# Performance work log

Hardware: AMD Instinct MI355X
Metric: run time of the kernel (lower is better)

## Reference

```python
import jax, jax.numpy as jnp
import numpy as np

S = 2          # scale_int = ceil(scale)
K = 3          # kernel size
OUTC = 3       # num_out_ch
NUM_FEAT = 64


def conv3x3(x, w, b):
    y = jax.lax.conv_general_dilated(x, w, (1, 1), ((1, 1), (1, 1)),
                                     dimension_numbers=('NCHW', 'OIHW', 'NCHW'))
    return y + b[None, :, None, None]


def unfold3x3(x):
    # torch F.unfold(x, 3, padding=1): (N, C*9, H*W), order c*9 + ki*3 + kj
    N, C, H, W = x.shape
    xp = jnp.pad(x, ((0, 0), (0, 0), (1, 1), (1, 1)))
    patches = jnp.stack([xp[:, :, i:i + H, j:j + W]
                         for i in range(3) for j in range(3)], axis=2)  # (N,C,9,H,W)
    return patches.reshape(N, C * 9, H * W)


def setup_inputs() -> dict:
    key = jax.random.key(0)
    ks = jax.random.split(key, 12)
    b, t, c, h, w = 2, 4, 16, 64, 64
    H, W = S * h, S * w
    nf4 = 64 // 4  # 16
    d_w = K * K * NUM_FEAT * OUTC  # 1728
    return {
        'x0': jax.random.normal(ks[0], (b, NUM_FEAT, h, w), jnp.float32),
        'feature': jax.random.normal(ks[1], (b, t, c, h, w), jnp.float32),
        'pos_mat': jax.random.uniform(ks[2], (H, W, 3), jnp.float32),
        'mask': jnp.ones((b, OUTC, H, W), dtype=bool),
        'conv1_w': jax.random.normal(ks[3], (nf4, 64, 3, 3), jnp.float32) * 0.05,
        'conv1_b': jnp.zeros((nf4,), jnp.float32),
        'conv2_w': jax.random.normal(ks[4], (nf4, nf4, 3, 3), jnp.float32) * 0.05,
        'conv2_b': jnp.zeros((nf4,), jnp.float32),
        'f2w1_w': jax.random.normal(ks[5], (256, nf4 + 1), jnp.float32) * 0.05,
        'f2w1_b': jnp.zeros((256,), jnp.float32),
        'f2w2_w': jax.random.normal(ks[6], (d_w, 256), jnp.float32) * 0.05,
        'f2w2_b': jnp.zeros((d_w,), jnp.float32),
    }


def reference(x0, feature, pos_mat, mask, conv1_w, conv1_b, conv2_w, conv2_b,
              f2w1_w, f2w1_b, f2w2_w, f2w2_b):
    b, t, c, h, w = feature.shape
    H, W = S * h, S * w
    # with_gradBack=False -> feature.detach()
    feat = jax.lax.stop_gradient(feature).reshape(b, t * c, h, w)
    # repeat_x(..., upsample=True): nearest-neighbour upsample by S
    feat_up = jnp.repeat(jnp.repeat(feat, S, axis=2), S, axis=3)  # (b,64,H,W)
    f = jax.nn.relu(conv3x3(feat_up, conv1_w, conv1_b))
    f = conv3x3(f, conv2_w, conv2_b)                              # (b,16,H,W)
    pos0 = jnp.transpose(pos_mat, (2, 0, 1))[0:1]                 # (1,H,W)
    fm = jnp.concatenate([f, jnp.broadcast_to(pos0[None], (b, 1, H, W))], axis=1)
    fm = fm.reshape(b, -1, H * W).transpose(0, 2, 1)              # (b,HW,17)
    hdn = jax.nn.relu(fm @ f2w1_w.T + f2w1_b)
    weights = hdn @ f2w2_w.T + f2w2_b                             # (b,HW,1728)
    weights = weights.reshape(b, h, S, w, S, K * K * NUM_FEAT, OUTC)
    weights = jnp.transpose(weights, (0, 2, 4, 1, 3, 5, 6))
    weights = weights.reshape(b, S * S, h * w, K * K * NUM_FEAT, OUTC)
    # repeat_x(x0) tiles x0 S^2 times -> all S^2 col copies identical; compute once
    cols = unfold3x3(x0).transpose(0, 2, 1)                       # (b,hw,576)
    out = jnp.einsum('bpk,bspko->bspo', cols, weights)            # (b,S^2,hw,3)
    out = jnp.transpose(out, (0, 1, 3, 2)).reshape(b, S, S, OUTC, h, w)
    out = jnp.transpose(out, (0, 3, 4, 1, 5, 2)).reshape(b, OUTC, H, W)
    # integer scale -> mask all True -> masked_select + view is identity
    return out, weights
```

## Files before the change

kernel.cpp:

```cpp
#include <hip/hip_runtime.h>

#define THREADS 256

#define Bsz 2
#define HWp 16384
#define Ntot (Bsz*HWp)
#define HID 256
#define Mm 1728
#define FMC 17
#define W_OFF 98304

#define F1_OFF  0
#define F1_SZ   (Bsz*16*HWp)
#define FM_OFF  F1_SZ
#define WB2_OFF (FM_OFF + Ntot*FMC)

typedef __attribute__((ext_vector_type(8))) short bf16x8;
typedef __attribute__((ext_vector_type(4))) float f32x4;

static __device__ __forceinline__ short f2bf(float x) {
    unsigned u = __builtin_bit_cast(unsigned, x);
    unsigned r = (u + 0x7fff + ((u >> 16) & 1)) >> 16;
    return (short)r;
}

__global__ __launch_bounds__(THREADS) void k13_conv1_cvt(const float* __restrict__ feat,
                                                         const float* __restrict__ w1,
                                                         const float* __restrict__ b1,
                                                         float* __restrict__ f1,
                                                         const float* __restrict__ w2g,
                                                         short* __restrict__ wB2) {
    int tid = threadIdx.x;
    if (blockIdx.x >= 256) {
        int t = (blockIdx.x - 256) * THREADS + tid;
        int i = t & 7, l = (t >> 3) & 63, ct = (t >> 9) & 3, s = (t >> 11) & 7, mc = t >> 14;
        int col = mc * 64 + ct * 16 + (l & 15);
        int k = s * 32 + (l >> 4) * 8 + i;
        wB2[t] = f2bf(w2g[col * HID + k]);
        return;
    }
    __shared__ float sW[4 * 64 * 4];
    int b = blockIdx.x;
    int rb = b & 7, oc = (b >> 3) & 15, bb = b >> 7;
    int c = tid & 63, sr = tid >> 6;
    int r0 = rb * 4 + sr;
    int r1 = r0 + 32;

    #pragma unroll
    for (int q = 0; q < 4; ++q) {
        int e = tid * 4 + q;
        int v = e & 1, u = (e >> 1) & 1, ic = (e >> 2) & 63, pp = (e >> 8) & 3;
        int pi = pp >> 1, pj = pp & 1;
        float s = 0.f;
        for (int ki = 0; ki < 3; ++ki) {
            bool okki = pi ? (u ? (ki == 2) : (ki <= 1)) : (u ? (ki >= 1) : (ki == 0));
            if (!okki) continue;
            for (int kj = 0; kj < 3; ++kj) {
                bool okkj = pj ? (v ? (kj == 2) : (kj <= 1)) : (v ? (kj >= 1) : (kj == 0));
                if (okkj) s += w1[((oc * 64 + ic) * 3 + ki) * 3 + kj];
            }
        }
        sW[(pp * 64 + ic) * 4 + u * 2 + v] = s;
    }
    __syncthreads();

    float bias = b1[oc];
    float aA00 = bias, aA01 = bias, aA10 = bias, aA11 = bias;
    float aB00 = bias, aB01 = bias, aB10 = bias, aB11 = bias;

    float mA = (r0 > 0) ? 1.f : 0.f;
    float mB = (r1 < 63) ? 1.f : 0.f;
    float mc0 = (c > 0) ? 1.f : 0.f, mc2 = (c < 63) ? 1.f : 0.f;
    int roA0 = (r0 > 0) ? -64 : 0;
    int roB2 = (r1 < 63) ? 64 : 0;
    int co0 = (c > 0) ? -1 : 0, co2 = (c < 63) ? 1 : 0;

    const float* fbA = feat + bb * 64 * 4096 + r0 * 64 + c;
    const float* fbB = feat + bb * 64 * 4096 + r1 * 64 + c;
    for (int ic = 0; ic < 64; ++ic) {
        const float* pA1 = fbA + ic * 4096;
        const float* pA0 = pA1 + roA0;
        const float* pA2 = pA1 + 64;
        const float* pB1 = fbB + ic * 4096;
        const float* pB0 = pB1 - 64;
        const float* pB2 = pB1 + roB2;

        float vA00 = pA0[co0] * (mA * mc0), vA01 = pA0[0] * mA, vA02 = pA0[co2] * (mA * mc2);
        float vA10 = pA1[co0] * mc0,        vA11 = pA1[0],      vA12 = pA1[co2] * mc2;
        float vA20 = pA2[co0] * mc0,        vA21 = pA2[0],      vA22 = pA2[co2] * mc2;
        float vB00 = pB0[co0] * mc0,        vB01 = pB0[0],      vB02 = pB0[co2] * mc2;
        float vB10 = pB1[co0] * mc0,        vB11 = pB1[0],      vB12 = pB1[co2] * mc2;
        float vB20 = pB2[co0] * (mB * mc0), vB21 = pB2[0] * mB, vB22 = pB2[co2] * (mB * mc2);

        f32x4 w0 = *(const f32x4*)(sW + (0 * 64 + ic) * 4);
        f32x4 w1v = *(const f32x4*)(sW + (1 * 64 + ic) * 4);
        f32x4 w2v = *(const f32x4*)(sW + (2 * 64 + ic) * 4);
        f32x4 w3 = *(const f32x4*)(sW + (3 * 64 + ic) * 4);

        aA00 = fmaf(w0[0], vA00, aA00); aA00 = fmaf(w0[1], vA01, aA00);
        aA00 = fmaf(w0[2], vA10, aA00); aA00 = fmaf(w0[3], vA11, aA00);
        aA01 = fmaf(w1v[0], vA01, aA01); aA01 = fmaf(w1v[1], vA02, aA01);
        aA01 = fmaf(w1v[2], vA11, aA01); aA01 = fmaf(w1v[3], vA12, aA01);
        aA10 = fmaf(w2v[0], vA10, aA10); aA10 = fmaf(w2v[1], vA11, aA10);
        aA10 = fmaf(w2v[2], vA20, aA10); aA10 = fmaf(w2v[3], vA21, aA10);
        aA11 = fmaf(w3[0], vA11, aA11); aA11 = fmaf(w3[1], vA12, aA11);
        aA11 = fmaf(w3[2], vA21, aA11); aA11 = fmaf(w3[3], vA22, aA11);

        aB00 = fmaf(w0[0], vB00, aB00); aB00 = fmaf(w0[1], vB01, aB00);
        aB00 = fmaf(w0[2], vB10, aB00); aB00 = fmaf(w0[3], vB11, aB00);
        aB01 = fmaf(w1v[0], vB01, aB01); aB01 = fmaf(w1v[1], vB02, aB01);
        aB01 = fmaf(w1v[2], vB11, aB01); aB01 = fmaf(w1v[3], vB12, aB01);
        aB10 = fmaf(w2v[0], vB10, aB10); aB10 = fmaf(w2v[1], vB11, aB10);
        aB10 = fmaf(w2v[2], vB20, aB10); aB10 = fmaf(w2v[3], vB21, aB10);
        aB11 = fmaf(w3[0], vB11, aB11); aB11 = fmaf(w3[1], vB12, aB11);
        aB11 = fmaf(w3[2], vB21, aB11); aB11 = fmaf(w3[3], vB22, aB11);
    }

    float* foA = f1 + (bb * 16 + oc) * HWp + (2 * r0) * 128 + 2 * c;
    *reinterpret_cast<float2*>(foA)       = make_float2(fmaxf(aA00, 0.f), fmaxf(aA01, 0.f));
    *reinterpret_cast<float2*>(foA + 128) = make_float2(fmaxf(aA10, 0.f), fmaxf(aA11, 0.f));
    float* foB = f1 + (bb * 16 + oc) * HWp + (2 * r1) * 128 + 2 * c;
    *reinterpret_cast<float2*>(foB)       = make_float2(fmaxf(aB00, 0.f), fmaxf(aB01, 0.f));
    *reinterpret_cast<float2*>(foB + 128) = make_float2(fmaxf(aB10, 0.f), fmaxf(aB11, 0.f));
}

__global__ __launch_bounds__(THREADS) void k2_conv2_fm(const float* __restrict__ f1,
                                                       const float* __restrict__ w2,
                                                       const float* __restrict__ b2,
                                                       const float* __restrict__ pos,
                                                       float* __restrict__ fm) {
    int tid = threadIdx.x;
    int t = blockIdx.x * THREADS + tid;
    int J = t & 127, I = (t >> 7) & 127, h = (t >> 14) & 1, bb = t >> 15;

    float acc[8];
    #pragma unroll
    for (int o = 0; o < 8; ++o) acc[o] = b2[h * 8 + o];

    int ro0 = (I > 0) ? -128 : 0, ro2 = (I < 127) ? 128 : 0;
    int co0 = (J > 0) ? -1 : 0, co2 = (J < 127) ? 1 : 0;
    float mr0 = (I > 0) ? 1.f : 0.f, mr2 = (I < 127) ? 1.f : 0.f;
    float mcl = (J > 0) ? 1.f : 0.f, mcr = (J < 127) ? 1.f : 0.f;

    const float* fb = f1 + bb * 16 * HWp + I * 128 + J;
    #pragma unroll 4
    for (int ic = 0; ic < 16; ++ic) {
        const float* p1 = fb + ic * HWp;
        const float* p0 = p1 + ro0;
        const float* p2 = p1 + ro2;
        float v0 = p0[co0] * (mr0 * mcl), v1 = p0[0] * mr0, v2 = p0[co2] * (mr0 * mcr);
        float v3 = p1[co0] * mcl,         v4 = p1[0],       v5 = p1[co2] * mcr;
        float v6 = p2[co0] * (mr2 * mcl), v7 = p2[0] * mr2, v8 = p2[co2] * (mr2 * mcr);
        const float* wp = w2 + (h * 8 * 16 + ic) * 9;
        #pragma unroll
        for (int o = 0; o < 8; ++o) {
            const float* w = wp + o * 144;
            acc[o] = fmaf(v0, w[0], acc[o]); acc[o] = fmaf(v1, w[1], acc[o]);
            acc[o] = fmaf(v2, w[2], acc[o]); acc[o] = fmaf(v3, w[3], acc[o]);
            acc[o] = fmaf(v4, w[4], acc[o]); acc[o] = fmaf(v5, w[5], acc[o]);
            acc[o] = fmaf(v6, w[6], acc[o]); acc[o] = fmaf(v7, w[7], acc[o]);
            acc[o] = fmaf(v8, w[8], acc[o]);
        }
    }
    int n = bb * HWp + I * 128 + J;
    #pragma unroll
    for (int o = 0; o < 8; ++o) fm[n * FMC + h * 8 + o] = acc[o];
    if (h == 0) fm[n * FMC + 16] = pos[(I * 128 + J) * 3];
}

__global__ __launch_bounds__(THREADS, 2) void k4_gemm(const float* __restrict__ fm,
                                                      const float* __restrict__ w1g,
                                                      const float* __restrict__ b1g,
                                                      const short* __restrict__ wB2,
                                                      const float* __restrict__ b2g,
                                                      const float* __restrict__ x0g,
                                                      float* __restrict__ dout) {
    __shared__ short    sA[16384];
    __shared__ float    sFM[64 * 20];
    __shared__ int      sOB[64];
    __shared__ float    sX[6528];
    __shared__ unsigned sLUT[1792];
    __shared__ float    sOut[4 * 64 * 3];

    int tid = threadIdx.x;
    int n0 = blockIdx.x * 64;
    int bb = n0 >> 14, tt = n0 & 16383, I = tt >> 7, J0 = tt & 127;
    int i0 = I >> 1, jmin = J0 >> 1;

    for (int idx = tid; idx < 64 * FMC; idx += THREADS) {
        int r = idx / FMC, i2 = idx - r * FMC;
        sFM[r * 20 + i2] = fm[n0 * FMC + idx];
    }
    if (tid < 64) {
        int J = J0 + tid;
        int s = ((I & 1) << 1) | (J & 1);
        int p = ((I >> 1) << 6) | (J >> 1);
        sOB[tid] = W_OFF + ((bb * 4 + s) * 4096 + p) * Mm;
    }
    for (int m = tid; m < Mm; m += THREADS) {
        int k = m / 3;
        int ch = k / 9, rem = k - ch * 9;
        int ki = rem / 3, kj = rem - ki * 3;
        sLUT[m] = (unsigned)((ch * 3 + ki) * 34 + kj);
    }
    {
        const float* x0b = x0g + bb * 64 * 4096;
        for (int e = tid; e < 6528; e += THREADS) {
            int ch = e / 102, r2 = e - ch * 102;
            int ki = r2 / 34, jc = r2 - ki * 34;
            int y = i0 + ki - 1, x = jmin + jc - 1;
            float v = 0.f;
            if ((unsigned)y < 64u && (unsigned)x < 64u) v = x0b[(ch * 64 + y) * 64 + x];
            sX[e] = v;
        }
    }
    __syncthreads();

    {
        float wreg[FMC];
        #pragma unroll
        for (int i = 0; i < FMC; ++i) wreg[i] = w1g[tid * FMC + i];
        float bj = b1g[tid];
        int g = (tid >> 3) & 7;
        int base = (tid >> 3) * 512 + (tid & 7);
        for (int rr = 0; rr < 64; ++rr) {
            int r = (rr + g) & 63;
            const float* fr = sFM + r * 20;
            f32x4 x0 = *(const f32x4*)fr;
            f32x4 x1 = *(const f32x4*)(fr + 4);
            f32x4 x2 = *(const f32x4*)(fr + 8);
            f32x4 x3 = *(const f32x4*)(fr + 12);
            float s = fmaf(fr[16], wreg[16], bj);
            s = fmaf(x0[0], wreg[0], s);  s = fmaf(x0[1], wreg[1], s);
            s = fmaf(x0[2], wreg[2], s);  s = fmaf(x0[3], wreg[3], s);
            s = fmaf(x1[0], wreg[4], s);  s = fmaf(x1[1], wreg[5], s);
            s = fmaf(x1[2], wreg[6], s);  s = fmaf(x1[3], wreg[7], s);
            s = fmaf(x2[0], wreg[8], s);  s = fmaf(x2[1], wreg[9], s);
            s = fmaf(x2[2], wreg[10], s); s = fmaf(x2[3], wreg[11], s);
            s = fmaf(x3[0], wreg[12], s); s = fmaf(x3[1], wreg[13], s);
            s = fmaf(x3[2], wreg[14], s); s = fmaf(x3[3], wreg[15], s);
            sA[base + r * 8] = f2bf(fmaxf(s, 0.f));
        }
    }
    __syncthreads();

    int wid = tid >> 6, l = tid & 63;
    int lm = l & 15, lg = l >> 4;
    int lg3 = lg % 3;

    int pixbase[4], jl[4];
    #pragma unroll
    for (int rt = 0; rt < 4; ++rt) {
        pixbase[rt] = sOB[rt * 16 + lm];
        jl[rt] = rt * 8 + (lm >> 1);
    }

    const short* aptr = sA + lg * 512 + lm * 8;

    float racc[4][3];
    #pragma unroll
    for (int rt = 0; rt < 4; ++rt) {
        racc[rt][0] = 0.f; racc[rt][1] = 0.f; racc[rt][2] = 0.f;
    }

    for (int mc = wid; mc < 27; mc += 4) {
        int m0 = mc * 64;
        f32x4 acc[4][4];
        #pragma unroll
        for (int ct = 0; ct < 4; ++ct) {
            f32x4 bias4 = *(const f32x4*)(b2g + m0 + ct * 16 + lg * 4);
            #pragma unroll
            for (int rt = 0; rt < 4; ++rt)
                acc[rt][ct] = bias4;
        }
        const short* bbase = wB2 + (size_t)mc * 16384 + l * 8;
        #pragma unroll 2
        for (int s = 0; s < 8; ++s) {
            bf16x8 af[4], bfr[4];
            #pragma unroll
            for (int rt = 0; rt < 4; ++rt)
                af[rt] = *(const bf16x8*)(aptr + s * 2048 + rt * 128);
            #pragma unroll
            for (int ct = 0; ct < 4; ++ct)
                bfr[ct] = *(const bf16x8*)(bbase + (s * 4 + ct) * 512);
            #pragma unroll
            for (int rt = 0; rt < 4; ++rt)
                #pragma unroll
                for (int ct = 0; ct < 4; ++ct)
                    acc[rt][ct] = __builtin_amdgcn_mfma_f32_16x16x32_bf16(
                        bfr[ct], af[rt], acc[rt][ct], 0, 0, 0);
        }
        #pragma unroll
        for (int rt = 0; rt < 4; ++rt)
            #pragma unroll
            for (int ct = 0; ct < 4; ++ct)
                *(f32x4*)(dout + pixbase[rt] + m0 + ct * 16 + lg * 4) = acc[rt][ct];
        unsigned lutv[4];
#define ACCUM(QB)                                                              \
        _Pragma("unroll")                                                      \
        for (int ct = 0; ct < 4; ++ct) {                                       \
            *(uint4*)lutv = *(const uint4*)(sLUT + m0 + ct * 16 + lg * 4);     \
            _Pragma("unroll")                                                  \
            for (int r = 0; r < 4; ++r) {                                      \
                _Pragma("unroll")                                              \
                for (int rt = 0; rt < 4; ++rt) {                               \
                    float v = sX[lutv[r] + jl[rt]];                            \
                    racc[rt][((QB) + ct + r) % 3] =                            \
                        fmaf(acc[rt][ct][r], v, racc[rt][((QB) + ct + r) % 3]);\
                }                                                              \
            }                                                                  \
        }
        switch (mc % 3) {
            case 0: ACCUM(0); break;
            case 1: ACCUM(1); break;
            default: ACCUM(2); break;
        }
#undef ACCUM
    }

    #pragma unroll
    for (int rt = 0; rt < 4; ++rt) {
        float q0 = racc[rt][0], q1 = racc[rt][1], q2 = racc[rt][2];
        float a0 = (lg3 == 0) ? q0 : ((lg3 == 1) ? q2 : q1);
        float a1 = (lg3 == 0) ? q1 : ((lg3 == 1) ? q0 : q2);
        float a2 = (lg3 == 0) ? q2 : ((lg3 == 1) ? q1 : q0);
        a0 += __shfl_xor(a0, 16, 64); a0 += __shfl_xor(a0, 32, 64);
        a1 += __shfl_xor(a1, 16, 64); a1 += __shfl_xor(a1, 32, 64);
        a2 += __shfl_xor(a2, 16, 64); a2 += __shfl_xor(a2, 32, 64);
        if (l < 16) {
            float* so = sOut + (wid * 64 + rt * 16 + lm) * 3;
            so[0] = a0; so[1] = a1; so[2] = a2;
        }
    }
    __syncthreads();
    if (tid < 192) {
        float s = sOut[tid] + sOut[192 + tid] + sOut[384 + tid] + sOut[576 + tid];
        int pix = tid / 3, o = tid - 3 * pix;
        dout[bb * 3 * HWp + o * HWp + I * 128 + J0 + pix] = s;
    }
}

extern "C" void kernel_launch(void* const* d_in, const int* in_sizes, int n_in,
                              void* d_out, int out_size, void* d_ws, size_t ws_size,
                              hipStream_t stream) {
    const float* x0      = (const float*)d_in[0];
    const float* feature = (const float*)d_in[1];
    const float* pos     = (const float*)d_in[2];
    const float* w1      = (const float*)d_in[4];
    const float* b1      = (const float*)d_in[5];
    const float* w2      = (const float*)d_in[6];
    const float* b2      = (const float*)d_in[7];
    const float* f2w1_w  = (const float*)d_in[8];
    const float* f2w1_b  = (const float*)d_in[9];
    const float* f2w2_w  = (const float*)d_in[10];
    const float* f2w2_b  = (const float*)d_in[11];

    float* out = (float*)d_out;
    float* ws  = (float*)d_ws;
    float* f1  = ws + F1_OFF;
    float* fm  = ws + FM_OFF;
    short* wB2 = (short*)(ws + WB2_OFF);

    k13_conv1_cvt<<<256 + 1728, THREADS, 0, stream>>>(feature, w1, b1, f1, f2w2_w, wB2);
    k2_conv2_fm<<<(Bsz * 2 * HWp) / THREADS, THREADS, 0, stream>>>(f1, w2, b2, pos, fm);
    k4_gemm<<<Ntot / 64, THREADS, 0, stream>>>(fm, f2w1_w, f2w1_b, wB2, f2w2_b, x0, out);
}
```

Before: 123.8 us.

## Split hidden layer into separate MFMA kernel staging bf16 activations in output buffer

Moves the first MLP layer (17->256 with ReLU) out of the main GEMM kernel into a new kernel that uses bf16 MFMA with a pre-converted, zero-padded weight tile. The bf16 hidden activations are written into the weights region of the output buffer as scratch and reloaded by the GEMM kernel with vector copies. The GEMM kernel also drops its LUT and restructures the x0 patch tile into a transposed layout, so the unfold indices are computed arithmetically with two loads per four outputs. This adds a kernel launch and a global round trip for the hidden activations. It depends on each block reading its scratch before other blocks overwrite that region, and the first-layer inputs and weights are now rounded to bf16.

```diff
diff --git a/kernel.cpp b/kernel.cpp
--- a/kernel.cpp
+++ b/kernel.cpp
@@ -14,6 +14,7 @@
 #define F1_SZ   (Bsz*16*HWp)
 #define FM_OFF  F1_SZ
 #define WB2_OFF (FM_OFF + Ntot*FMC)
+#define WB1_OFF (WB2_OFF + (Mm*HID)/2)
 
 typedef __attribute__((ext_vector_type(8))) short bf16x8;
 typedef __attribute__((ext_vector_type(4))) float f32x4;
@@ -29,8 +30,18 @@
                                                          const float* __restrict__ b1,
                                                          float* __restrict__ f1,
                                                          const float* __restrict__ w2g,
-                                                         short* __restrict__ wB2) {
+                                                         short* __restrict__ wB2,
+                                                         const float* __restrict__ w1g,
+                                                         short* __restrict__ wB1) {
     int tid = threadIdx.x;
+    if (blockIdx.x >= 1984) {
+        for (int idx = tid; idx < 8192; idx += THREADS) {
+            int i = idx & 7, l = (idx >> 3) & 63, h = idx >> 9;
+            int k = (l >> 4) * 8 + i, hid = h * 16 + (l & 15);
+            wB1[idx] = (k < FMC) ? f2bf(w1g[hid * FMC + k]) : (short)0;
+        }
+        return;
+    }
     if (blockIdx.x >= 256) {
         int t = (blockIdx.x - 256) * THREADS + tid;
         int i = t & 7, l = (t >> 3) & 63, ct = (t >> 9) & 3, s = (t >> 11) & 7, mc = t >> 14;
@@ -168,40 +179,71 @@
     if (h == 0) fm[n * FMC + 16] = pos[(I * 128 + J) * 3];
 }
 
-__global__ __launch_bounds__(THREADS, 2) void k4_gemm(const float* __restrict__ fm,
-                                                      const float* __restrict__ w1g,
-                                                      const float* __restrict__ b1g,
-                                                      const short* __restrict__ wB2,
+__global__ __launch_bounds__(THREADS) void k35_hdn(const float* __restrict__ fm,
+                                                   const short* __restrict__ wB1,
+                                                   const float* __restrict__ b1g,
+                                                   float* __restrict__ dout) {
+    int tid = threadIdx.x;
+    int n0 = blockIdx.x * 64;
+    int bb = n0 >> 14, tt = n0 & 16383, I = tt >> 7, J0 = tt & 127;
+    int s0 = (I & 1) * 2, i0 = I >> 1, jmin = J0 >> 1;
+    short* sp = (short*)(dout + (size_t)W_OFF +
+                         ((size_t)(bb * 4 + s0) * 4096 + i0 * 64 + jmin) * Mm);
+
+    int w = tid >> 6, l = tid & 63, lm = l & 15, lg = l >> 4;
+    int row = w * 16 + lm;
+    const float* fr = fm + (n0 + row) * FMC;
+    bf16x8 af;
+    #pragma unroll
+    for (int i = 0; i < 8; ++i) {
+        int k = lg * 8 + i;
+        float x = (k < FMC) ? fr[k] : 0.f;
+        af[i] = f2bf(x);
+    }
+    const short* wb = wB1 + l * 8;
+    int pbase = ((lg >> 1) * 64 + row) * 8 + (lg & 1) * 4;
+    #pragma unroll 4
+    for (int h = 0; h < 16; ++h) {
+        bf16x8 bfr = *(const bf16x8*)(wb + h * 512);
+        f32x4 bias = *(const f32x4*)(b1g + h * 16 + lg * 4);
+        f32x4 acc = __builtin_amdgcn_mfma_f32_16x16x32_bf16(bfr, af, bias, 0, 0, 0);
+        unsigned c0 = (unsigned short)f2bf(fmaxf(acc[0], 0.f));
+        unsigned c1 = (unsigned short)f2bf(fmaxf(acc[1], 0.f));
+        unsigned c2 = (unsigned short)f2bf(fmaxf(acc[2], 0.f));
+        unsigned c3 = (unsigned short)f2bf(fmaxf(acc[3], 0.f));
+        uint2 uv; uv.x = c0 | (c1 << 16); uv.y = c2 | (c3 << 16);
+        *(uint2*)(sp + pbase + h * 1024) = uv;
+    }
+}
+
+__global__ __launch_bounds__(THREADS, 2) void k4_gemm(const short* __restrict__ wB2,
                                                       const float* __restrict__ b2g,
                                                       const float* __restrict__ x0g,
                                                       float* __restrict__ dout) {
-    __shared__ short    sA[16384];
-    __shared__ float    sFM[64 * 20];
-    __shared__ int      sOB[64];
-    __shared__ float    sX[6528];
-    __shared__ unsigned sLUT[1792];
-    __shared__ float    sOut[4 * 64 * 3];
+    __shared__ short sA[16384];
+    __shared__ int   sOB[64];
+    __shared__ float sXT[6632];
+    __shared__ float sOut[4 * 64 * 3];
 
     int tid = threadIdx.x;
     int n0 = blockIdx.x * 64;
     int bb = n0 >> 14, tt = n0 & 16383, I = tt >> 7, J0 = tt & 127;
-    int i0 = I >> 1, jmin = J0 >> 1;
-
-    for (int idx = tid; idx < 64 * FMC; idx += THREADS) {
-        int r = idx / FMC, i2 = idx - r * FMC;
-        sFM[r * 20 + i2] = fm[n0 * FMC + idx];
+    int s0 = (I & 1) * 2, i0 = I >> 1, jmin = J0 >> 1;
+
+    {
+        const short* spc = (const short*)(dout + (size_t)W_OFF +
+                             ((size_t)(bb * 4 + s0) * 4096 + i0 * 64 + jmin) * Mm);
+        #pragma unroll
+        for (int q = 0; q < 8; ++q) {
+            int si = (q * 256 + tid) * 8;
+            *(bf16x8*)(sA + si) = *(const bf16x8*)(spc + si);
+        }
     }
     if (tid < 64) {
         int J = J0 + tid;
         int s = ((I & 1) << 1) | (J & 1);
         int p = ((I >> 1) << 6) | (J >> 1);
         sOB[tid] = W_OFF + ((bb * 4 + s) * 4096 + p) * Mm;
-    }
-    for (int m = tid; m < Mm; m += THREADS) {
-        int k = m / 3;
-        int ch = k / 9, rem = k - ch * 9;
-        int ki = rem / 3, kj = rem - ki * 3;
-        sLUT[m] = (unsigned)((ch * 3 + ki) * 34 + kj);
     }
     {
         const float* x0b = x0g + bb * 64 * 4096;
@@ -211,48 +253,20 @@
             int y = i0 + ki - 1, x = jmin + jc - 1;
             float v = 0.f;
             if ((unsigned)y < 64u && (unsigned)x < 64u) v = x0b[(ch * 64 + y) * 64 + x];
-            sX[e] = v;
-        }
-    }
-    __syncthreads();
-
-    {
-        float wreg[FMC];
-        #pragma unroll
-        for (int i = 0; i < FMC; ++i) wreg[i] = w1g[tid * FMC + i];
-        float bj = b1g[tid];
-        int g = (tid >> 3) & 7;
-        int base = (tid >> 3) * 512 + (tid & 7);
-        for (int rr = 0; rr < 64; ++rr) {
-            int r = (rr + g) & 63;
-            const float* fr = sFM + r * 20;
-            f32x4 x0 = *(const f32x4*)fr;
-            f32x4 x1 = *(const f32x4*)(fr + 4);
-            f32x4 x2 = *(const f32x4*)(fr + 8);
-            f32x4 x3 = *(const f32x4*)(fr + 12);
-            float s = fmaf(fr[16], wreg[16], bj);
-            s = fmaf(x0[0], wreg[0], s);  s = fmaf(x0[1], wreg[1], s);
-            s = fmaf(x0[2], wreg[2], s);  s = fmaf(x0[3], wreg[3], s);
-            s = fmaf(x1[0], wreg[4], s);  s = fmaf(x1[1], wreg[5], s);
-            s = fmaf(x1[2], wreg[6], s);  s = fmaf(x1[3], wreg[7], s);
-            s = fmaf(x2[0], wreg[8], s);  s = fmaf(x2[1], wreg[9], s);
-            s = fmaf(x2[2], wreg[10], s); s = fmaf(x2[3], wreg[11], s);
-            s = fmaf(x3[0], wreg[12], s); s = fmaf(x3[1], wreg[13], s);
-            s = fmaf(x3[2], wreg[14], s); s = fmaf(x3[3], wreg[15], s);
-            sA[base + r * 8] = f2bf(fmaxf(s, 0.f));
+            sXT[jc * 195 + ch * 3 + ki] = v;
         }
     }
     __syncthreads();
 
     int wid = tid >> 6, l = tid & 63;
     int lm = l & 15, lg = l >> 4;
-    int lg3 = lg % 3;
-
-    int pixbase[4], jl[4];
+    int lg3 = lg % 3, lg4 = lg * 4;
+
+    int pixbase[4], jl195[4];
     #pragma unroll
     for (int rt = 0; rt < 4; ++rt) {
         pixbase[rt] = sOB[rt * 16 + lm];
-        jl[rt] = rt * 8 + (lm >> 1);
+        jl195[rt] = (rt * 8 + (lm >> 1)) * 195;
     }
 
     const short* aptr = sA + lg * 512 + lm * 8;
@@ -295,19 +309,30 @@
             #pragma unroll
             for (int ct = 0; ct < 4; ++ct)
                 *(f32x4*)(dout + pixbase[rt] + m0 + ct * 16 + lg * 4) = acc[rt][ct];
-        unsigned lutv[4];
 #define ACCUM(QB)                                                              \
         _Pragma("unroll")                                                      \
         for (int ct = 0; ct < 4; ++ct) {                                       \
-            *(uint4*)lutv = *(const uint4*)(sLUT + m0 + ct * 16 + lg * 4);     \
+            int t = m0 + ct * 16 + lg4;                                        \
+            int K0 = (t * 21846) >> 16;                                        \
+            int rem3 = t - 3 * K0;                                             \
+            int Q2 = (K0 * 21846) >> 16;                                       \
+            int kja = K0 - 3 * Q2;                                             \
+            int kqa = kja * 195 + Q2;                                          \
+            int kqb = (kja == 2) ? (Q2 + 1) : (kqa + 195);                     \
             _Pragma("unroll")                                                  \
-            for (int r = 0; r < 4; ++r) {                                      \
-                _Pragma("unroll")                                              \
-                for (int rt = 0; rt < 4; ++rt) {                               \
-                    float v = sX[lutv[r] + jl[rt]];                            \
-                    racc[rt][((QB) + ct + r) % 3] =                            \
-                        fmaf(acc[rt][ct][r], v, racc[rt][((QB) + ct + r) % 3]);\
-                }                                                              \
+            for (int rt = 0; rt < 4; ++rt) {                                   \
+                float xa = sXT[jl195[rt] + kqa];                               \
+                float xb = sXT[jl195[rt] + kqb];                               \
+                float x1 = (rem3 == 2) ? xb : xa;                              \
+                float x2 = (rem3 >= 1) ? xb : xa;                              \
+                racc[rt][(QB + ct) % 3] =                                      \
+                    fmaf(acc[rt][ct][0], xa, racc[rt][(QB + ct) % 3]);         \
+                racc[rt][(QB + ct + 1) % 3] =                                  \
+                    fmaf(acc[rt][ct][1], x1, racc[rt][(QB + ct + 1) % 3]);     \
+                racc[rt][(QB + ct + 2) % 3] =                                  \
+                    fmaf(acc[rt][ct][2], x2, racc[rt][(QB + ct + 2) % 3]);     \
+                racc[rt][(QB + ct) % 3] =                                      \
+                    fmaf(acc[rt][ct][3], xb, racc[rt][(QB + ct) % 3]);         \
             }                                                                  \
         }
         switch (mc % 3) {
@@ -360,8 +385,11 @@
     float* f1  = ws + F1_OFF;
     float* fm  = ws + FM_OFF;
     short* wB2 = (short*)(ws + WB2_OFF);
-
-    k13_conv1_cvt<<<256 + 1728, THREADS, 0, stream>>>(feature, w1, b1, f1, f2w2_w, wB2);
+    short* wB1 = (short*)(ws + WB1_OFF);
+
+    k13_conv1_cvt<<<1985, THREADS, 0, stream>>>(feature, w1, b1, f1, f2w2_w, wB2,
+                                                f2w1_w, wB1);
     k2_conv2_fm<<<(Bsz * 2 * HWp) / THREADS, THREADS, 0, stream>>>(f1, w2, b2, pos, fm);
-    k4_gemm<<<Ntot / 64, THREADS, 0, stream>>>(fm, f2w1_w, f2w1_b, wB2, f2w2_b, x0, out);
-}
+    k35_hdn<<<Ntot / 64, THREADS, 0, stream>>>(fm, wB1, f2w1_b, out);
+    k4_gemm<<<Ntot / 64, THREADS, 0, stream>>>(wB2, f2w2_b, x0, out);
+}
```

New measurement: 126.5 us. +2.2%, slower.
